# Optimization experiments

Hardware: AMD Instinct MI355X
Metric: run time of the kernel (lower is better)

Reference implementation:

```python
import jax, jax.numpy as jnp
import numpy as np

B, S, D, H, DH, F = 4, 2048, 1024, 16, 64, 4096
EPS = 1e-5


def setup_inputs() -> dict:
    key = jax.random.key(0)
    ks = jax.random.split(key, 8)
    std = 0.02
    return {
        "src": jax.random.normal(ks[0], (B, S, D), dtype=jnp.float32),
        # per-head Q/K/V projections, stacked: [H, D, DH]
        "Wq": jax.random.normal(ks[1], (H, D, DH), dtype=jnp.float32) * std,
        "bq": jnp.zeros((H, DH), dtype=jnp.float32),
        "Wk": jax.random.normal(ks[2], (H, D, DH), dtype=jnp.float32) * std,
        "bk": jnp.zeros((H, DH), dtype=jnp.float32),
        "Wv": jax.random.normal(ks[3], (H, D, DH), dtype=jnp.float32) * std,
        "bv": jnp.zeros((H, DH), dtype=jnp.float32),
        "Wo": jax.random.normal(ks[4], (H * DH, D), dtype=jnp.float32) * std,
        "bo": jnp.zeros((D,), dtype=jnp.float32),
        "ln1_w": jnp.ones((D,), dtype=jnp.float32),
        "ln1_b": jnp.zeros((D,), dtype=jnp.float32),
        "W1": jax.random.normal(ks[5], (D, F), dtype=jnp.float32) * std,
        "b1": jnp.zeros((F,), dtype=jnp.float32),
        "W2": jax.random.normal(ks[6], (F, D), dtype=jnp.float32) * std,
        "b2": jnp.zeros((D,), dtype=jnp.float32),
        "ln2_w": jnp.ones((D,), dtype=jnp.float32),
        "ln2_b": jnp.zeros((D,), dtype=jnp.float32),
    }


def _layernorm(x, w, b):
    m = jnp.mean(x, axis=-1, keepdims=True)
    v = jnp.mean(jnp.square(x - m), axis=-1, keepdims=True)
    return (x - m) * jax.lax.rsqrt(v + EPS) * w + b


def reference(src, Wq, bq, Wk, bk, Wv, bv, Wo, bo, ln1_w, ln1_b, W1, b1, W2, b2, ln2_w, ln2_b):
    # Per-head projections, batched over heads: [B,H,S,DH]
    q = jnp.einsum('bsd,hde->bhse', src, Wq) + bq[None, :, None, :]
    k = jnp.einsum('bsd,hde->bhse', src, Wk) + bk[None, :, None, :]
    v = jnp.einsum('bsd,hde->bhse', src, Wv) + bv[None, :, None, :]
    scale = jnp.asarray(DH, src.dtype) ** 0.5
    scores = jnp.einsum('bhqe,bhke->bhqk', q, k) / scale  # [B,H,S,S]
    attn = jax.nn.softmax(scores, axis=-1)
    ctx = jnp.einsum('bhqk,bhke->bhqe', attn, v)  # [B,H,S,DH]
    # concat heads along feature dim (matches torch.cat over head outputs)
    ctx = ctx.transpose(0, 2, 1, 3).reshape(src.shape[0], src.shape[1], H * DH)
    attn_out = ctx @ Wo + bo
    x = _layernorm(src + attn_out, ln1_w, ln1_b)
    ffn = jax.nn.relu(x @ W1 + b1) @ W2 + b2
    return _layernorm(x + ffn, ln2_w, ln2_b)
```

## Files before the change

### kernel.cpp

```cpp
#include <hip/hip_runtime.h>
#include <stdint.h>


typedef unsigned short u16;
typedef __attribute__((ext_vector_type(8))) short short8;
typedef __attribute__((ext_vector_type(4))) float f32x4;

__device__ __forceinline__ u16 f2bf(float f) {
  union { float f; unsigned u; } v; v.f = f;
  unsigned r = (v.u + 0x7fffu + ((v.u >> 16) & 1u)) >> 16;
  return (u16)r;
}

__device__ __forceinline__ unsigned pack_trunc(float f0, float f1) {
  union { float f; unsigned u; } a, b;
  a.f = f0; b.f = f1;
  return __builtin_amdgcn_perm(b.u, a.u, 0x07060302u);
}

__device__ __forceinline__ void gl_lds16(const u16* g, u16* l) {
  __builtin_amdgcn_global_load_lds(
      (const __attribute__((address_space(1))) unsigned int*)g,
      (__attribute__((address_space(3))) unsigned int*)l, 16, 0, 0);
}


__global__ __launch_bounds__(256) void transpose_cast(const float* __restrict__ W,
                                                      u16* __restrict__ WT,
                                                      int K, int N) {
  __shared__ u16 T[64 * 72];
  const int tid = threadIdx.x;
  const long n0 = (long)blockIdx.x * 64, k0 = (long)blockIdx.y * 64;
#pragma unroll
  for (int i = 0; i < 4; i++) {
    int c = tid + i * 256;
    int kr = c >> 4, nc = (c & 15) * 4;
    float4 v = *(const float4*)(W + (k0 + kr) * N + n0 + nc);
    T[(nc + 0) * 72 + kr] = f2bf(v.x);
    T[(nc + 1) * 72 + kr] = f2bf(v.y);
    T[(nc + 2) * 72 + kr] = f2bf(v.z);
    T[(nc + 3) * 72 + kr] = f2bf(v.w);
  }
  __syncthreads();
#pragma unroll
  for (int i = 0; i < 2; i++) {
    int c = tid + i * 256;
    int nr = c >> 3, kc = (c & 7) * 8;
    *(uint4*)(WT + (n0 + nr) * K + k0 + kc) = *(const uint4*)(T + nr * 72 + kc);
  }
}

__global__ __launch_bounds__(256) void transpose_cast_qkv(const float* __restrict__ Wq,
                                                          const float* __restrict__ Wk,
                                                          const float* __restrict__ Wv,
                                                          u16* __restrict__ WT) {
  __shared__ u16 T[64 * 72];
  const int tid = threadIdx.x;
  const int n0 = blockIdx.x * 64, k0 = blockIdx.y * 64;
  const float* W = (n0 < 1024) ? Wq : (n0 < 2048 ? Wk : Wv);
  const int h = (n0 & 1023) >> 6;
#pragma unroll
  for (int i = 0; i < 4; i++) {
    int c = tid + i * 256;
    int kr = c >> 4, ec = (c & 15) * 4;
    float4 v = *(const float4*)(W + ((long)h * 1024 + k0 + kr) * 64 + ec);
    T[(ec + 0) * 72 + kr] = f2bf(v.x);
    T[(ec + 1) * 72 + kr] = f2bf(v.y);
    T[(ec + 2) * 72 + kr] = f2bf(v.z);
    T[(ec + 3) * 72 + kr] = f2bf(v.w);
  }
  __syncthreads();
#pragma unroll
  for (int i = 0; i < 2; i++) {
    int c = tid + i * 256;
    int nr = c >> 3, kc = (c & 7) * 8;
    *(uint4*)(WT + ((long)(n0 + nr)) * 1024 + k0 + kc) = *(const uint4*)(T + nr * 72 + kc);
  }
}

__global__ __launch_bounds__(256) void cast_bf16(const float* __restrict__ x, u16* __restrict__ y) {
  const long i = ((long)blockIdx.x * 256 + threadIdx.x) * 8;
  float4 a = *(const float4*)(x + i);
  float4 b = *(const float4*)(x + i + 4);
  uint4 o;
  o.x = (unsigned)f2bf(a.x) | ((unsigned)f2bf(a.y) << 16);
  o.y = (unsigned)f2bf(a.z) | ((unsigned)f2bf(a.w) << 16);
  o.z = (unsigned)f2bf(b.x) | ((unsigned)f2bf(b.y) << 16);
  o.w = (unsigned)f2bf(b.z) | ((unsigned)f2bf(b.w) << 16);
  *(uint4*)(y + i) = o;
}

__global__ __launch_bounds__(256) void build_bcat(const float* __restrict__ bq,
                                                  const float* __restrict__ bk,
                                                  const float* __restrict__ bv,
                                                  float* __restrict__ bcat) {
  int i = blockIdx.x * 256 + threadIdx.x;
  const float* s = (i < 1024) ? bq : (i < 2048 ? bk : bv);
  bcat[i] = s[i & 1023];
}

#define GEMM_PROLOGUE                                                            \
  __shared__ __align__(16) u16 As[128 * 32];                                     \
  __shared__ __align__(16) u16 Bs[128 * 32];                                     \
  const int tid = threadIdx.x;                                                   \
  const int wave = tid >> 6, lane = tid & 63, quad = lane >> 4, l15 = lane & 15; \
  const int wm = (wave >> 1) * 64, wn = (wave & 1) * 64;                         \
  const long m0 = (long)blockIdx.y * 128, n0 = (long)blockIdx.x * 128;           \
  const u16* Ag = A + (m0 + (tid >> 2)) * K + (tid & 3) * 8;                     \
  const u16* Bg = B + (n0 + (tid >> 2)) * K + (tid & 3) * 8;                     \
  u16* Asl = As + tid * 8;                                                       \
  u16* Bsl = Bs + tid * 8;                                                       \
  f32x4 acc[4][4] = {};                                                          \
  for (int k0 = 0; k0 < K; k0 += 32) {                                           \
    __syncthreads();                                                             \
    gl_lds16(Ag + k0, Asl);                                                      \
    gl_lds16(Ag + (long)64 * K + k0, Asl + 2048);                                \
    gl_lds16(Bg + k0, Bsl);                                                      \
    gl_lds16(Bg + (long)64 * K + k0, Bsl + 2048);                                \
    __syncthreads();                                                             \
    short8 af[4], bfr[4];                                                        \
    _Pragma("unroll") for (int t = 0; t < 4; t++)                                \
        af[t] = *(const short8*)(As + (wm + t * 16 + l15) * 32 + quad * 8);      \
    _Pragma("unroll") for (int t = 0; t < 4; t++)                                \
        bfr[t] = *(const short8*)(Bs + (wn + t * 16 + l15) * 32 + quad * 8);     \
    _Pragma("unroll") for (int i = 0; i < 4; i++)                                \
        _Pragma("unroll") for (int j = 0; j < 4; j++)                            \
            acc[i][j] = __builtin_amdgcn_mfma_f32_16x16x32_bf16(af[i], bfr[j],   \
                                                                acc[i][j], 0, 0, 0); \
  }

template <int MODE>
__global__ __launch_bounds__(256) void gemm_bt(const u16* __restrict__ A, const u16* __restrict__ B,
                                               const float* __restrict__ bias, void* __restrict__ Cout,
                                               int K, int N) {
  GEMM_PROLOGUE
#pragma unroll
  for (int i = 0; i < 4; i++) {
#pragma unroll
    for (int j = 0; j < 4; j++) {
      const long col = n0 + wn + j * 16 + l15;
      const float bb = bias[col];
      const long rowb = m0 + wm + i * 16 + quad * 4;
#pragma unroll
      for (int r = 0; r < 4; r++) {
        float v = acc[i][j][r] + bb;
        if (MODE == 2) v = fmaxf(v, 0.f);
        if (MODE == 0)
          ((float*)Cout)[(rowb + r) * N + col] = v;
        else
          ((u16*)Cout)[(rowb + r) * N + col] = f2bf(v);
      }
    }
  }
}

__global__ __launch_bounds__(256) void gemm_qkv(const u16* __restrict__ A, const u16* __restrict__ B,
                                                const float* __restrict__ bias,
                                                u16* __restrict__ QKb, u16* __restrict__ Vt, int K) {
  GEMM_PROLOGUE
#pragma unroll
  for (int i = 0; i < 4; i++) {
#pragma unroll
    for (int j = 0; j < 4; j++) {
      const int col0 = (int)n0 + wn + j * 16;
      const int col = col0 + l15;
      const float bb = bias[col];
      const long rowb = m0 + wm + i * 16 + quad * 4;
      if (col0 < 1024) {
#pragma unroll
        for (int r = 0; r < 4; r++)
          QKb[(rowb + r) * 2048 + col] = f2bf((acc[i][j][r] + bb) * 0.1803368801f);
      } else if (col0 < 2048) {
#pragma unroll
        for (int r = 0; r < 4; r++)
          QKb[(rowb + r) * 2048 + col] = f2bf(acc[i][j][r] + bb);
      } else {
        const int ec = col - 2048;
        const int bq = (int)(rowb >> 11), s = (int)(rowb & 2047);
        uint2 p;
        p.x = (unsigned)f2bf(acc[i][j][0] + bb) | ((unsigned)f2bf(acc[i][j][1] + bb) << 16);
        p.y = (unsigned)f2bf(acc[i][j][2] + bb) | ((unsigned)f2bf(acc[i][j][3] + bb) << 16);
        *(uint2*)(Vt + ((long)(bq * 16 + (ec >> 6)) * 64 + (ec & 63)) * 2048 + s) = p;
      }
    }
  }
}

#define PSLD 68

__device__ __forceinline__ void stage_tile(const u16* __restrict__ g, u16* __restrict__ lds, int tid) {
#pragma unroll
  for (int i = 0; i < 2; i++) {
    const int s = i * 256 + tid;
    const int r = s >> 3, cs = s & 7;
    const int c = cs ^ (r & 7);
    gl_lds16(g + (long)r * 2048 + c * 8, lds + s * 8);
  }
}
__device__ __forceinline__ short8 frag(const u16* __restrict__ buf, int row, int chunk) {
  const int slot = row * 8 + (chunk ^ (row & 7));
  return *(const short8*)(buf + slot * 8);
}

__global__ __launch_bounds__(256, 2) void flash_attn(const u16* __restrict__ QKb,
                                                     const u16* __restrict__ Vt,
                                                     u16* __restrict__ ctx) {
  __shared__ __align__(16) u16 Kbuf[2][4096];
  __shared__ __align__(16) u16 Vbuf[2][4096];
  __shared__ u16 Ps[8 * 16 * PSLD];
  const int tid = threadIdx.x, wave = tid >> 6, lane = tid & 63, quad = lane >> 4, l15 = lane & 15;
  const int bh = blockIdx.y, b = bh >> 4, h = bh & 15;
  const int qt = blockIdx.x;
  const u16* Qg = QKb + ((long)b * 2048 + qt * 128 + wave * 32) * 2048 + h * 64;
  const u16* Kg = QKb + ((long)b * 2048) * 2048 + 1024 + h * 64;
  const u16* Vg = Vt + (long)bh * 64 * 2048;

  short8 qf[2][2];
#pragma unroll
  for (int u = 0; u < 2; u++)
#pragma unroll
    for (int ks = 0; ks < 2; ks++)
      qf[u][ks] = *(const short8*)(Qg + (long)(u * 16 + l15) * 2048 + ks * 32 + quad * 8);

  f32x4 O[2][4] = {};
  f32x4 Os[2] = {};
  const short8 ones = {0x3F80, 0x3F80, 0x3F80, 0x3F80, 0x3F80, 0x3F80, 0x3F80, 0x3F80};
  u16* myP[2];
#pragma unroll
  for (int u = 0; u < 2; u++) myP[u] = Ps + ((wave * 2 + u) * 16 + l15) * PSLD;

  stage_tile(Kg, Kbuf[0], tid);
  stage_tile(Vg, Vbuf[0], tid);

  for (int kt = 0; kt < 32; kt++) {
    __syncthreads();
    if (kt < 31) {
      stage_tile(Kg + (long)(kt + 1) * 64 * 2048, Kbuf[(kt + 1) & 1], tid);
      stage_tile(Vg + (kt + 1) * 64, Vbuf[(kt + 1) & 1], tid);
    }
    const u16* Kb = Kbuf[kt & 1];
    const u16* Vb = Vbuf[kt & 1];

    f32x4 S[2][4];
#pragma unroll
    for (int m = 0; m < 4; m++) {
      const short8 a0 = frag(Kb, m * 16 + l15, quad);
      const short8 a1 = frag(Kb, m * 16 + l15, 4 + quad);
#pragma unroll
      for (int u = 0; u < 2; u++) {
        f32x4 s = {0.f, 0.f, 0.f, 0.f};
        s = __builtin_amdgcn_mfma_f32_16x16x32_bf16(a0, qf[u][0], s, 0, 0, 0);
        s = __builtin_amdgcn_mfma_f32_16x16x32_bf16(a1, qf[u][1], s, 0, 0, 0);
        S[u][m] = s;
      }
    }

#pragma unroll
    for (int u = 0; u < 2; u++)
#pragma unroll
      for (int m = 0; m < 4; m++) {
#pragma unroll
        for (int r = 0; r < 4; r++) S[u][m][r] = __builtin_amdgcn_exp2f(S[u][m][r]);
        uint2 p;
        p.x = pack_trunc(S[u][m][0], S[u][m][1]);
        p.y = pack_trunc(S[u][m][2], S[u][m][3]);
        *(uint2*)(myP[u] + m * 16 + quad * 4) = p;
      }
    short8 pf[2][2];
#pragma unroll
    for (int u = 0; u < 2; u++) {
      pf[u][0] = *(const short8*)(myP[u] + quad * 8);
      pf[u][1] = *(const short8*)(myP[u] + 32 + quad * 8);
      Os[u] = __builtin_amdgcn_mfma_f32_16x16x32_bf16(ones, pf[u][0], Os[u], 0, 0, 0);
      Os[u] = __builtin_amdgcn_mfma_f32_16x16x32_bf16(ones, pf[u][1], Os[u], 0, 0, 0);
    }

#pragma unroll
    for (int et = 0; et < 4; et++) {
      const short8 v0 = frag(Vb, et * 16 + l15, quad);
      const short8 v1 = frag(Vb, et * 16 + l15, 4 + quad);
#pragma unroll
      for (int u = 0; u < 2; u++) {
        O[u][et] = __builtin_amdgcn_mfma_f32_16x16x32_bf16(v0, pf[u][0], O[u][et], 0, 0, 0);
        O[u][et] = __builtin_amdgcn_mfma_f32_16x16x32_bf16(v1, pf[u][1], O[u][et], 0, 0, 0);
      }
    }
  }

#pragma unroll
  for (int u = 0; u < 2; u++) {
    const float inv = 1.f / Os[u][0];
    const long row = (long)b * 2048 + qt * 128 + wave * 32 + u * 16 + l15;
#pragma unroll
    for (int et = 0; et < 4; et++) {
      uint2 p;
      p.x = (unsigned)f2bf(O[u][et][0] * inv) | ((unsigned)f2bf(O[u][et][1] * inv) << 16);
      p.y = (unsigned)f2bf(O[u][et][2] * inv) | ((unsigned)f2bf(O[u][et][3] * inv) << 16);
      *(uint2*)(ctx + row * 1024 + h * 64 + et * 16 + quad * 4) = p;
    }
  }
}

template <bool WB>
__global__ __launch_bounds__(256) void add_ln(const float* __restrict__ a, const float* __restrict__ c,
                                              const float* __restrict__ w, const float* __restrict__ bias,
                                              float* __restrict__ xout, u16* __restrict__ xbf) {
  const int row = blockIdx.x, tid = threadIdx.x;
  const long off = (long)row * 1024 + tid * 4;
  float4 va = *(const float4*)(a + off);
  float4 vc = *(const float4*)(c + off);
  float4 s = {va.x + vc.x, va.y + vc.y, va.z + vc.z, va.w + vc.w};
  float sum = s.x + s.y + s.z + s.w;
  float sq = s.x * s.x + s.y * s.y + s.z * s.z + s.w * s.w;
#pragma unroll
  for (int o = 32; o > 0; o >>= 1) {
    sum += __shfl_xor(sum, o);
    sq += __shfl_xor(sq, o);
  }
  __shared__ float red[8];
  const int wave = tid >> 6;
  if ((tid & 63) == 0) { red[wave] = sum; red[wave + 4] = sq; }
  __syncthreads();
  sum = red[0] + red[1] + red[2] + red[3];
  sq = red[4] + red[5] + red[6] + red[7];
  const float mean = sum * (1.f / 1024.f);
  const float var = sq * (1.f / 1024.f) - mean * mean;
  const float rstd = rsqrtf(var + 1e-5f);
  float4 vw = *(const float4*)(w + tid * 4);
  float4 vb = *(const float4*)(bias + tid * 4);
  float4 y;
  y.x = (s.x - mean) * rstd * vw.x + vb.x;
  y.y = (s.y - mean) * rstd * vw.y + vb.y;
  y.z = (s.z - mean) * rstd * vw.z + vb.z;
  y.w = (s.w - mean) * rstd * vw.w + vb.w;
  *(float4*)(xout + off) = y;
  if (WB) {
    uint2 o2;
    o2.x = (unsigned)f2bf(y.x) | ((unsigned)f2bf(y.y) << 16);
    o2.y = (unsigned)f2bf(y.z) | ((unsigned)f2bf(y.w) << 16);
    *(uint2*)(xbf + off) = o2;
  }
}

extern "C" void kernel_launch(void* const* d_in, const int* in_sizes, int n_in,
                              void* d_out, int out_size, void* d_ws, size_t ws_size,
                              hipStream_t stream) {
  (void)in_sizes; (void)n_in; (void)out_size; (void)ws_size;
  const float* src = (const float*)d_in[0];
  const float* Wq = (const float*)d_in[1];
  const float* bq = (const float*)d_in[2];
  const float* Wk = (const float*)d_in[3];
  const float* bk = (const float*)d_in[4];
  const float* Wv = (const float*)d_in[5];
  const float* bv = (const float*)d_in[6];
  const float* Wo = (const float*)d_in[7];
  const float* bo = (const float*)d_in[8];
  const float* ln1w = (const float*)d_in[9];
  const float* ln1b = (const float*)d_in[10];
  const float* W1 = (const float*)d_in[11];
  const float* b1 = (const float*)d_in[12];
  const float* W2 = (const float*)d_in[13];
  const float* b2 = (const float*)d_in[14];
  const float* ln2w = (const float*)d_in[15];
  const float* ln2b = (const float*)d_in[16];

  char* ws = (char*)d_ws;
  u16* WqkvT = (u16*)(ws + 0);
  u16* WoT = (u16*)(ws + (6ul << 20));
  u16* W1T = (u16*)(ws + (8ul << 20));
  u16* W2T = (u16*)(ws + (16ul << 20));
  float* bcat = (float*)(ws + (24ul << 20));
  u16* srcb = (u16*)(ws + (25ul << 20));
  u16* QKb = (u16*)(ws + (41ul << 20));
  u16* Vt = (u16*)(ws + (73ul << 20));
  u16* ctxb = (u16*)(ws + (89ul << 20));
  float* x = (float*)(ws + (105ul << 20));
  u16* xb = (u16*)(ws + (137ul << 20));
  u16* hb = (u16*)(ws + (41ul << 20));
  float* out = (float*)d_out;

  transpose_cast_qkv<<<dim3(48, 16), 256, 0, stream>>>(Wq, Wk, Wv, WqkvT);
  transpose_cast<<<dim3(16, 16), 256, 0, stream>>>(Wo, WoT, 1024, 1024);
  transpose_cast<<<dim3(64, 16), 256, 0, stream>>>(W1, W1T, 1024, 4096);
  transpose_cast<<<dim3(16, 64), 256, 0, stream>>>(W2, W2T, 4096, 1024);
  cast_bf16<<<4096, 256, 0, stream>>>(src, srcb);
  build_bcat<<<12, 256, 0, stream>>>(bq, bk, bv, bcat);

  gemm_qkv<<<dim3(24, 64), 256, 0, stream>>>(srcb, WqkvT, bcat, QKb, Vt, 1024);
  flash_attn<<<dim3(16, 64), 256, 0, stream>>>(QKb, Vt, ctxb);
  gemm_bt<0><<<dim3(8, 64), 256, 0, stream>>>(ctxb, WoT, bo, out, 1024, 1024);
  add_ln<true><<<8192, 256, 0, stream>>>(src, out, ln1w, ln1b, x, xb);
  gemm_bt<2><<<dim3(32, 64), 256, 0, stream>>>(xb, W1T, b1, hb, 1024, 4096);
  gemm_bt<0><<<dim3(8, 64), 256, 0, stream>>>(hb, W2T, b2, out, 4096, 1024);
  add_ln<false><<<8192, 256, 0, stream>>>(x, out, ln2w, ln2b, out, nullptr);
}
```

Before: 621.2 us.

## Double flash-attention query tile to 256 rows and reorder grid by head

Each wave now handles 64 query rows instead of 32, so every staged K/V tile in LDS serves twice as many queries and global K/V traffic is halved. The grid is also transposed so blocks sharing the same batch-head are adjacent, which should improve L2 reuse of K/V. The P scratch buffer is reused across two halves to keep LDS size unchanged. The cost is more accumulator registers (O grows to 4x4 f32x4), which may hurt occupancy under launch_bounds(256,2), and only 512 blocks are launched.

```diff
diff --git a/kernel.cpp b/kernel.cpp
--- a/kernel.cpp
+++ b/kernel.cpp
@@ -209,21 +209,21 @@
   __shared__ __align__(16) u16 Vbuf[2][4096];
   __shared__ u16 Ps[8 * 16 * PSLD];
   const int tid = threadIdx.x, wave = tid >> 6, lane = tid & 63, quad = lane >> 4, l15 = lane & 15;
-  const int bh = blockIdx.y, b = bh >> 4, h = bh & 15;
-  const int qt = blockIdx.x;
-  const u16* Qg = QKb + ((long)b * 2048 + qt * 128 + wave * 32) * 2048 + h * 64;
+  const int bh = blockIdx.x, b = bh >> 4, h = bh & 15;
+  const int qt = blockIdx.y;
+  const u16* Qg = QKb + ((long)b * 2048 + qt * 256 + wave * 64) * 2048 + h * 64;
   const u16* Kg = QKb + ((long)b * 2048) * 2048 + 1024 + h * 64;
   const u16* Vg = Vt + (long)bh * 64 * 2048;
 
-  short8 qf[2][2];
-#pragma unroll
-  for (int u = 0; u < 2; u++)
+  short8 qf[4][2];
+#pragma unroll
+  for (int u = 0; u < 4; u++)
 #pragma unroll
     for (int ks = 0; ks < 2; ks++)
       qf[u][ks] = *(const short8*)(Qg + (long)(u * 16 + l15) * 2048 + ks * 32 + quad * 8);
 
-  f32x4 O[2][4] = {};
-  f32x4 Os[2] = {};
+  f32x4 O[4][4] = {};
+  f32x4 Os[4] = {};
   const short8 ones = {0x3F80, 0x3F80, 0x3F80, 0x3F80, 0x3F80, 0x3F80, 0x3F80, 0x3F80};
   u16* myP[2];
 #pragma unroll
@@ -241,38 +241,42 @@
     const u16* Kb = Kbuf[kt & 1];
     const u16* Vb = Vbuf[kt & 1];
 
-    f32x4 S[2][4];
-#pragma unroll
-    for (int m = 0; m < 4; m++) {
-      const short8 a0 = frag(Kb, m * 16 + l15, quad);
-      const short8 a1 = frag(Kb, m * 16 + l15, 4 + quad);
-#pragma unroll
-      for (int u = 0; u < 2; u++) {
-        f32x4 s = {0.f, 0.f, 0.f, 0.f};
-        s = __builtin_amdgcn_mfma_f32_16x16x32_bf16(a0, qf[u][0], s, 0, 0, 0);
-        s = __builtin_amdgcn_mfma_f32_16x16x32_bf16(a1, qf[u][1], s, 0, 0, 0);
-        S[u][m] = s;
+    short8 pf[4][2];
+#pragma unroll
+    for (int half = 0; half < 2; half++) {
+      f32x4 S[2][4];
+#pragma unroll
+      for (int m = 0; m < 4; m++) {
+        const short8 a0 = frag(Kb, m * 16 + l15, quad);
+        const short8 a1 = frag(Kb, m * 16 + l15, 4 + quad);
+#pragma unroll
+        for (int uu = 0; uu < 2; uu++) {
+          f32x4 s = {0.f, 0.f, 0.f, 0.f};
+          s = __builtin_amdgcn_mfma_f32_16x16x32_bf16(a0, qf[half * 2 + uu][0], s, 0, 0, 0);
+          s = __builtin_amdgcn_mfma_f32_16x16x32_bf16(a1, qf[half * 2 + uu][1], s, 0, 0, 0);
+          S[uu][m] = s;
+        }
       }
-    }
-
-#pragma unroll
-    for (int u = 0; u < 2; u++)
-#pragma unroll
-      for (int m = 0; m < 4; m++) {
-#pragma unroll
-        for (int r = 0; r < 4; r++) S[u][m][r] = __builtin_amdgcn_exp2f(S[u][m][r]);
-        uint2 p;
-        p.x = pack_trunc(S[u][m][0], S[u][m][1]);
-        p.y = pack_trunc(S[u][m][2], S[u][m][3]);
-        *(uint2*)(myP[u] + m * 16 + quad * 4) = p;
+
+#pragma unroll
+      for (int uu = 0; uu < 2; uu++)
+#pragma unroll
+        for (int m = 0; m < 4; m++) {
+#pragma unroll
+          for (int r = 0; r < 4; r++) S[uu][m][r] = __builtin_amdgcn_exp2f(S[uu][m][r]);
+          uint2 p;
+          p.x = pack_trunc(S[uu][m][0], S[uu][m][1]);
+          p.y = pack_trunc(S[uu][m][2], S[uu][m][3]);
+          *(uint2*)(myP[uu] + m * 16 + quad * 4) = p;
+        }
+#pragma unroll
+      for (int uu = 0; uu < 2; uu++) {
+        const int u = half * 2 + uu;
+        pf[u][0] = *(const short8*)(myP[uu] + quad * 8);
+        pf[u][1] = *(const short8*)(myP[uu] + 32 + quad * 8);
+        Os[u] = __builtin_amdgcn_mfma_f32_16x16x32_bf16(ones, pf[u][0], Os[u], 0, 0, 0);
+        Os[u] = __builtin_amdgcn_mfma_f32_16x16x32_bf16(ones, pf[u][1], Os[u], 0, 0, 0);
       }
-    short8 pf[2][2];
-#pragma unroll
-    for (int u = 0; u < 2; u++) {
-      pf[u][0] = *(const short8*)(myP[u] + quad * 8);
-      pf[u][1] = *(const short8*)(myP[u] + 32 + quad * 8);
-      Os[u] = __builtin_amdgcn_mfma_f32_16x16x32_bf16(ones, pf[u][0], Os[u], 0, 0, 0);
-      Os[u] = __builtin_amdgcn_mfma_f32_16x16x32_bf16(ones, pf[u][1], Os[u], 0, 0, 0);
     }
 
 #pragma unroll
@@ -280,7 +284,7 @@
       const short8 v0 = frag(Vb, et * 16 + l15, quad);
       const short8 v1 = frag(Vb, et * 16 + l15, 4 + quad);
 #pragma unroll
-      for (int u = 0; u < 2; u++) {
+      for (int u = 0; u < 4; u++) {
         O[u][et] = __builtin_amdgcn_mfma_f32_16x16x32_bf16(v0, pf[u][0], O[u][et], 0, 0, 0);
         O[u][et] = __builtin_amdgcn_mfma_f32_16x16x32_bf16(v1, pf[u][1], O[u][et], 0, 0, 0);
       }
@@ -288,9 +292,9 @@
   }
 
 #pragma unroll
-  for (int u = 0; u < 2; u++) {
+  for (int u = 0; u < 4; u++) {
     const float inv = 1.f / Os[u][0];
-    const long row = (long)b * 2048 + qt * 128 + wave * 32 + u * 16 + l15;
+    const long row = (long)b * 2048 + qt * 256 + wave * 64 + u * 16 + l15;
 #pragma unroll
     for (int et = 0; et < 4; et++) {
       uint2 p;
@@ -387,7 +391,7 @@
   build_bcat<<<12, 256, 0, stream>>>(bq, bk, bv, bcat);
 
   gemm_qkv<<<dim3(24, 64), 256, 0, stream>>>(srcb, WqkvT, bcat, QKb, Vt, 1024);
-  flash_attn<<<dim3(16, 64), 256, 0, stream>>>(QKb, Vt, ctxb);
+  flash_attn<<<dim3(64, 8), 256, 0, stream>>>(QKb, Vt, ctxb);
   gemm_bt<0><<<dim3(8, 64), 256, 0, stream>>>(ctxb, WoT, bo, out, 1024, 1024);
   add_ln<true><<<8192, 256, 0, stream>>>(src, out, ln1w, ln1b, x, xb);
   gemm_bt<2><<<dim3(32, 64), 256, 0, stream>>>(xb, W1T, b1, hb, 1024, 4096);
```

Result: faster. 604.4 us (-2.7%).
